# Optimization experiments

Measured on AMD Instinct MI355X. Metric: run time of the kernel, lower is better.

Reference implementation:

```python
import jax, jax.numpy as jnp
import numpy as np

K = 3
TAPS = K * K
STD = float(np.sqrt(2.0)) / K  # FilterNorm scale: relu gain / kernel_size


def filter_norm(f, axis):
    # torch FilterNorm: subtract mean, divide by unbiased std (+1e-10), scale by STD
    m = jnp.mean(f, axis=axis, keepdims=True)
    sd = jnp.std(f, axis=axis, keepdims=True, ddof=1)
    return (f - m) / (sd + 1e-10) * STD


def setup_inputs() -> dict:
    key = jax.random.key(0)
    ks = jax.random.split(key, 9)
    B, C, H, W = 4, 64, 192, 192
    mid = int(C * 0.2)  # se_ratio=0.2 -> 12
    f = lambda k, shape, s: jax.random.normal(k, shape, jnp.float32) * s
    return {
        'x':   f(ks[0], (B, C, H, W), 1.0),
        'sw':  f(ks[1], (TAPS, C), 0.05),        # spatial branch 1x1 conv weight
        'sb':  f(ks[2], (TAPS,), 0.05),
        'cw1': f(ks[3], (mid, C), 0.05),         # channel branch squeeze
        'cb1': f(ks[4], (mid,), 0.05),
        'cw2': f(ks[5], (C * TAPS, mid), 0.05),  # channel branch expand
        'cb2': f(ks[6], (C * TAPS,), 0.05),
        'w2':  f(ks[7], (C, C, 1, 9), 0.05),     # trailing 1x9 conv
        'b2':  f(ks[8], (C,), 0.05),
    }


def block_forward(x, sw, sb, cw1, cb1, cw2, cb2, w2, b2):
    B, C, H, W = x.shape
    # --- DDFPack ---
    # spatial filters: 1x1 conv -> (B, 9, H, W), FilterNorm across the 9 taps
    s = jnp.einsum('bchw,tc->bthw', x, sw) + sb[None, :, None, None]
    s = filter_norm(s, axis=1)
    # channel filters: GAP -> 1x1 -> relu -> 1x1 -> (B, C, 9), FilterNorm over taps
    g = x.mean(axis=(2, 3))                         # (B, C)
    h1 = jax.nn.relu(g @ cw1.T + cb1)               # (B, mid)
    cf = (h1 @ cw2.T + cb2).reshape(B, C, TAPS)     # (B, C, 9)
    cf = filter_norm(cf, axis=2)
    # decoupled dynamic filter apply: per-pixel depthwise 3x3, combine='mul', pad=1
    xp = jnp.pad(x, ((0, 0), (0, 0), (1, 1), (1, 1)))
    out = jnp.zeros_like(x)
    for idx in range(TAPS):  # fixed 9-tap loop, no big unfold intermediate
        i, j = idx // K, idx % K
        out = out + xp[:, :, i:i + H, j:j + W] * s[:, idx:idx + 1] * cf[:, :, idx, None, None]
    # --- LeakyReLU(0.1) -> 1x9 conv (pad (0,4)) -> residual add (res_scale=1) ---
    a = jnp.where(out >= 0, out, 0.1 * out)
    y = jax.lax.conv_general_dilated(a, w2, (1, 1), ((0, 0), (4, 4)),
                                     dimension_numbers=('NCHW', 'OIHW', 'NCHW'))
    y = y + b2[None, :, None, None]
    return x + y


def reference(x, sw, sb, cw1, cb1, cw2, cb2, w2, b2):
    return block_forward(x, sw, sb, cw1, cb1, cw2, cb2, w2, b2)
```

## Files before the change

kernel.cpp:

```cpp
#include <hip/hip_runtime.h>
#include <hip/hip_bf16.h>

#define B_    4
#define C_    64
#define H_    192
#define W_    192
#define TAPS_ 9
#define MID_  12
#define HW_   (H_ * W_)
#define K_TOT 576
#define AT_STRIDE 72

constexpr float STD_ = 0.47140452079103173f;

using bf16 = __hip_bfloat16;
typedef __attribute__((ext_vector_type(4))) float  f32x4;
typedef __attribute__((ext_vector_type(8))) short  short8;

__device__ __forceinline__ unsigned short f2bf_bits(float v) {
    union { bf16 h; unsigned short u; } cv;
    cv.h = __float2bfloat16(v);
    return cv.u;
}

__device__ __forceinline__ int at_word(int row, int cw) {
    int key = (row >> 2) & 7;
    return row * (AT_STRIDE / 2) + ((((cw >> 2) ^ key) & 7) << 2) + (cw & 3);
}

__global__ __launch_bounds__(256) void k_pre(const float* __restrict__ x,
                                             const float* __restrict__ w2,
                                             unsigned short* __restrict__ w2bf,
                                             float* __restrict__ partials) {
    int bx = blockIdx.x;
    if (bx < 144) {
        int d = bx * 256 + threadIdx.x;
        int o = d / K_TOT;
        int rem = d - o * K_TOT;
        int t = rem >> 6;
        int c = rem & 63;
        w2bf[d] = f2bf_bits(w2[(o * C_ + c) * TAPS_ + t]);
        return;
    }
    bx -= 144;
    int bc = bx / 3, part = bx - 3 * (bx / 3);
    const float4* p = (const float4*)(x + (size_t)bc * HW_ + part * 12288);
    float s = 0.f;
    #pragma unroll
    for (int k = 0; k < 12; ++k) {
        float4 u = p[threadIdx.x + k * 256];
        s += u.x + u.y + u.z + u.w;
    }
    #pragma unroll
    for (int off = 32; off; off >>= 1) s += __shfl_down(s, off);
    __shared__ float red[4];
    if ((threadIdx.x & 63) == 0) red[threadIdx.x >> 6] = s;
    __syncthreads();
    if (threadIdx.x == 0)
        partials[bx] = red[0] + red[1] + red[2] + red[3];
}

__global__ __launch_bounds__(256) void k_cf(const float* __restrict__ partials,
                                            const float* __restrict__ cw1,
                                            const float* __restrict__ cb1,
                                            const float* __restrict__ cw2,
                                            const float* __restrict__ cb2,
                                            float* __restrict__ cfn) {
    __shared__ float g_l[B_ * C_];
    __shared__ float h1_l[B_ * MID_];
    int tid = threadIdx.x;
    g_l[tid] = (partials[tid * 3] + partials[tid * 3 + 1] + partials[tid * 3 + 2])
               * (1.0f / HW_);
    __syncthreads();
    if (tid < B_ * MID_) {
        int b = tid / MID_, m = tid % MID_;
        float acc = cb1[m];
        for (int c = 0; c < C_; ++c) acc += g_l[b * C_ + c] * cw1[m * C_ + c];
        h1_l[tid] = fmaxf(acc, 0.f);
    }
    __syncthreads();
    int b = tid >> 6, c = tid & 63;
    float f[TAPS_];
    float mean = 0.f;
    #pragma unroll
    for (int t = 0; t < TAPS_; ++t) {
        int n = c * TAPS_ + t;
        float acc = cb2[n];
        #pragma unroll
        for (int m = 0; m < MID_; ++m) acc += h1_l[b * MID_ + m] * cw2[n * MID_ + m];
        f[t] = acc;
        mean += acc;
    }
    mean *= (1.f / TAPS_);
    float var = 0.f;
    #pragma unroll
    for (int t = 0; t < TAPS_; ++t) { float d = f[t] - mean; var += d * d; }
    var *= (1.f / (TAPS_ - 1));
    float scale = STD_ / (sqrtf(fmaxf(var, 0.f)) + 1e-10f);
    #pragma unroll
    for (int t = 0; t < TAPS_; ++t)
        cfn[(b * C_ + c) * TAPS_ + t] = (f[t] - mean) * scale;
}

__global__ __launch_bounds__(256, 3) void k_main(const float* __restrict__ x,
                                                 const float* __restrict__ sw,
                                                 const float* __restrict__ sb,
                                                 const float* __restrict__ cfn,
                                                 const unsigned short* __restrict__ w2bf,
                                                 const float* __restrict__ bias2,
                                                 float* __restrict__ out) {
    __shared__ __align__(16) char smem[36016];
    short*          aT   = (short*)smem;
    unsigned*       aT32 = (unsigned*)smem;
    float*          sw_l = (float*)smem;
    float*          s_l  = (float*)(smem + 28800);
    float*          b2_l = (float*)(smem + 35712);
    float*          sb_l = (float*)(smem + 35968);

    int bh = blockIdx.x;
    int bb = bh / H_;
    int h  = bh - bb * H_;
    int tid = threadIdx.x;
    int lane = tid & 63, wid = tid >> 6;
    int quad = lane >> 4, l16 = lane & 15;
    int obase = wid * 16;

    for (int i = tid; i < TAPS_ * C_; i += 256) sw_l[i] = sw[i];
    if (tid < C_) b2_l[tid] = bias2[tid];
    if (tid < TAPS_) sb_l[tid] = sb[tid];
    __syncthreads();

    const short* w2s = (const short*)w2bf;
    const short* arow = w2s + (obase + l16) * K_TOT + quad * 8;
    short8 a0 = *(const short8*)(arow);
    short8 a1 = *(const short8*)(arow + 32);

    if (tid < W_) {
        int w = tid;
        float acc[TAPS_];
        #pragma unroll
        for (int t = 0; t < TAPS_; ++t) acc[t] = sb_l[t];
        const float* px = x + (size_t)bb * C_ * HW_ + h * W_ + w;
        #pragma unroll 8
        for (int c = 0; c < C_; ++c) {
            float xv = px[(size_t)c * HW_];
            #pragma unroll
            for (int t = 0; t < TAPS_; ++t) acc[t] = fmaf(xv, sw_l[t * C_ + c], acc[t]);
        }
        float mean = 0.f;
        #pragma unroll
        for (int t = 0; t < TAPS_; ++t) mean += acc[t];
        mean *= (1.f / TAPS_);
        float var = 0.f;
        #pragma unroll
        for (int t = 0; t < TAPS_; ++t) { float d = acc[t] - mean; var += d * d; }
        var *= (1.f / (TAPS_ - 1));
        float scale = STD_ / (sqrtf(fmaxf(var, 0.f)) + 1e-10f);
        float* sp = s_l + (w & 3) * 432 + (w >> 2);
        #pragma unroll
        for (int t = 0; t < TAPS_; ++t) sp[t * 48] = (acc[t] - mean) * scale;
    }
    __syncthreads();

    for (int i = tid; i < 8 * (AT_STRIDE / 2); i += 256) {
        int rowIdx = i / (AT_STRIDE / 2);
        int col    = i - rowIdx * (AT_STRIDE / 2);
        int r = (rowIdx < 4) ? rowIdx : (192 + rowIdx);
        aT32[r * (AT_STRIDE / 2) + col] = 0u;
    }

    {
        int wbase = wid * 16;
        if (lane < 48) {
            int w0 = 4 * lane;
            float sreg[4][TAPS_];
            #pragma unroll
            for (int k = 0; k < 4; ++k) {
                const float* sp = s_l + k * 432 + lane;
                #pragma unroll
                for (int t = 0; t < TAPS_; ++t) sreg[k][t] = sp[t * 48];
            }
            bool l0 = (lane == 0), l47 = (lane == 47);
            int rok0 = (h > 0), rok2 = (h < H_ - 1);
            int midx = l0 ? 0 : (w0 - 1);
            int pidx = l47 ? w0 : (w0 + 4);
            const float* xbase = x + (long)bb * C_ * HW_ + (long)(h - 1) * W_;
            #pragma unroll 1
            for (int i = 0; i < 16; i += 2) {
                int c0 = wbase + i;
                int cu = __builtin_amdgcn_readfirstlane(c0);
                const float* cfp = cfn + bb * (C_ * TAPS_) + cu * TAPS_;
                const float* pc0 = xbase + (long)c0 * HW_;
                const float* pc1 = pc0 + HW_;
                float acc0[4] = {0.f, 0.f, 0.f, 0.f};
                float acc1[4] = {0.f, 0.f, 0.f, 0.f};
                #pragma unroll
                for (int r = 0; r < 3; ++r) {
                    if (r == 0 && !rok0) continue;
                    if (r == 2 && !rok2) continue;
                    const float* p0 = pc0 + r * W_;
                    const float* p1 = pc1 + r * W_;
                    float4 fa = *(const float4*)(p0 + w0);
                    float4 fb = *(const float4*)(p1 + w0);
                    float ma = l0 ? 0.f : p0[midx];
                    float mb = l0 ? 0.f : p1[midx];
                    float pa = l47 ? 0.f : p0[pidx];
                    float pb = l47 ? 0.f : p1[pidx];
                    float va[6] = { ma, fa.x, fa.y, fa.z, fa.w, pa };
                    float vb[6] = { mb, fb.x, fb.y, fb.z, fb.w, pb };
                    #pragma unroll
                    for (int dc = 0; dc < 3; ++dc) {
                        int t = r * 3 + dc;
                        float cva = cfp[t];
                        float cvb = cfp[TAPS_ + t];
                        #pragma unroll
                        for (int k = 0; k < 4; ++k) {
                            acc0[k] = fmaf(va[k + dc] * sreg[k][t], cva, acc0[k]);
                            acc1[k] = fmaf(vb[k + dc] * sreg[k][t], cvb, acc1[k]);
                        }
                    }
                }
                int cw = c0 >> 1;
                #pragma unroll
                for (int k = 0; k < 4; ++k) {
                    float a0v = acc0[k]; a0v = (a0v >= 0.f) ? a0v : 0.1f * a0v;
                    float a1v = acc1[k]; a1v = (a1v >= 0.f) ? a1v : 0.1f * a1v;
                    unsigned pk = (unsigned)f2bf_bits(a0v)
                                | ((unsigned)f2bf_bits(a1v) << 16);
                    aT32[at_word(w0 + k + 4, cw)] = pk;
                }
            }
        }
    }
    __syncthreads();

    {
        f32x4 acc[12];
        #pragma unroll
        for (int n = 0; n < 12; ++n) acc[n] = (f32x4){0.f, 0.f, 0.f, 0.f};

        #pragma unroll 1
        for (int kk = 0; kk < 18; ++kk) {
            short8 a2 = a1;
            if (kk < 16) a2 = *(const short8*)(arow + (kk + 2) * 32);
            int t = kk >> 1;
            int ch = ((kk & 1) << 2) + quad;
            int rowb = l16 + t;
            int key0 = (rowb >> 2) & 7;
            int off0 = rowb * AT_STRIDE + (((ch ^ key0) & 7) << 3);
            int off1 = rowb * AT_STRIDE + (((ch ^ key0 ^ 4) & 7) << 3);
            #pragma unroll
            for (int n = 0; n < 12; ++n) {
                int off = ((n & 1) ? off1 : off0) + n * 16 * AT_STRIDE;
                short8 bf = *(const short8*)(aT + off);
                acc[n] = __builtin_amdgcn_mfma_f32_16x16x32_bf16(a0, bf, acc[n], 0, 0, 0);
            }
            a0 = a1; a1 = a2;
        }

        size_t xbase = (size_t)bb * C_ * HW_ + (size_t)h * W_;
        #pragma unroll
        for (int n = 0; n < 12; ++n) {
            int w = n * 16 + l16;
            #pragma unroll
            for (int reg = 0; reg < 4; ++reg) {
                int o = obase + quad * 4 + reg;
                size_t idx = xbase + (size_t)o * HW_ + w;
                out[idx] = acc[n][reg] + b2_l[o] + x[idx];
            }
        }
    }
}

extern "C" void kernel_launch(void* const* d_in, const int* in_sizes, int n_in,
                              void* d_out, int out_size, void* d_ws, size_t ws_size,
                              hipStream_t stream) {
    const float* x   = (const float*)d_in[0];
    const float* sw  = (const float*)d_in[1];
    const float* sb  = (const float*)d_in[2];
    const float* cw1 = (const float*)d_in[3];
    const float* cb1 = (const float*)d_in[4];
    const float* cw2 = (const float*)d_in[5];
    const float* cb2 = (const float*)d_in[6];
    const float* w2  = (const float*)d_in[7];
    const float* b2  = (const float*)d_in[8];
    float* out = (float*)d_out;

    unsigned short* w2bf = (unsigned short*)d_ws;
    float* partials = (float*)((char*)d_ws + 73728);
    float* cfn      = (float*)((char*)d_ws + 76800);

    hipLaunchKernelGGL(k_pre, dim3(912), dim3(256), 0, stream, x, w2, w2bf, partials);
    hipLaunchKernelGGL(k_cf, dim3(1), dim3(256), 0, stream,
                       partials, cw1, cb1, cw2, cb2, cfn);
    hipLaunchKernelGGL(k_main, dim3(B_ * H_), dim3(256), 0, stream,
                       x, sw, sb, cfn, w2bf, b2, out);
}
```

Before: 147.9 us.

## Retile MFMA stage, prefetch depthwise rows, use lane shuffles for halo

The 1x9 conv MFMA stage now gives each wave two 16-row output-channel tiles by six width tiles, instead of one 16-row tile by twelve width tiles. Each B fragment read from LDS is reused for two MFMAs, which halves LDS traffic per MFMA. The depthwise stage software-prefetches the next channel pair's three input rows into registers and gets the left/right halo values through lane shuffles rather than extra scalar global loads. The weight-conversion pre-kernel is rewritten to read w2 contiguously and scatter the writes, and the 1x1 spatial loop unroll goes from 8 to 16. These changes raise register pressure, which could reduce occupancy.

```diff
diff --git a/kernel.cpp b/kernel.cpp
--- a/kernel.cpp
+++ b/kernel.cpp
@@ -34,12 +34,12 @@
                                              float* __restrict__ partials) {
     int bx = blockIdx.x;
     if (bx < 144) {
-        int d = bx * 256 + threadIdx.x;
-        int o = d / K_TOT;
-        int rem = d - o * K_TOT;
-        int t = rem >> 6;
-        int c = rem & 63;
-        w2bf[d] = f2bf_bits(w2[(o * C_ + c) * TAPS_ + t]);
+        int s = bx * 256 + threadIdx.x;
+        int o = s / K_TOT;
+        int rem = s - o * K_TOT;
+        int c = rem / TAPS_;
+        int t = rem - c * TAPS_;
+        w2bf[o * K_TOT + t * 64 + c] = f2bf_bits(w2[s]);
         return;
     }
     bx -= 144;
@@ -123,7 +123,8 @@
     int tid = threadIdx.x;
     int lane = tid & 63, wid = tid >> 6;
     int quad = lane >> 4, l16 = lane & 15;
-    int obase = wid * 16;
+    int opair = wid & 1;
+    int nh    = wid >> 1;
 
     for (int i = tid; i < TAPS_ * C_; i += 256) sw_l[i] = sw[i];
     if (tid < C_) b2_l[tid] = bias2[tid];
@@ -131,9 +132,12 @@
     __syncthreads();
 
     const short* w2s = (const short*)w2bf;
-    const short* arow = w2s + (obase + l16) * K_TOT + quad * 8;
-    short8 a0 = *(const short8*)(arow);
-    short8 a1 = *(const short8*)(arow + 32);
+    const short* arowA = w2s + (opair * 32 + l16) * K_TOT + quad * 8;
+    const short* arowB = arowA + 16 * K_TOT;
+    short8 aA0 = *(const short8*)(arowA);
+    short8 aA1 = *(const short8*)(arowA + 32);
+    short8 aB0 = *(const short8*)(arowB);
+    short8 aB1 = *(const short8*)(arowB + 32);
 
     if (tid < W_) {
         int w = tid;
@@ -141,7 +145,7 @@
         #pragma unroll
         for (int t = 0; t < TAPS_; ++t) acc[t] = sb_l[t];
         const float* px = x + (size_t)bb * C_ * HW_ + h * W_ + w;
-        #pragma unroll 8
+        #pragma unroll 16
         for (int c = 0; c < C_; ++c) {
             float xv = px[(size_t)c * HW_];
             #pragma unroll
@@ -182,32 +186,48 @@
             }
             bool l0 = (lane == 0), l47 = (lane == 47);
             int rok0 = (h > 0), rok2 = (h < H_ - 1);
-            int midx = l0 ? 0 : (w0 - 1);
-            int pidx = l47 ? w0 : (w0 + 4);
             const float* xbase = x + (long)bb * C_ * HW_ + (long)(h - 1) * W_;
+            const float4 z4 = {0.f, 0.f, 0.f, 0.f};
+
+            float4 nf[6];
+            {
+                const float* pc0 = xbase + (long)wbase * HW_;
+                const float* pc1 = pc0 + HW_;
+                nf[0] = rok0 ? *(const float4*)(pc0 + w0) : z4;
+                nf[1] = *(const float4*)(pc0 + W_ + w0);
+                nf[2] = rok2 ? *(const float4*)(pc0 + 2 * W_ + w0) : z4;
+                nf[3] = rok0 ? *(const float4*)(pc1 + w0) : z4;
+                nf[4] = *(const float4*)(pc1 + W_ + w0);
+                nf[5] = rok2 ? *(const float4*)(pc1 + 2 * W_ + w0) : z4;
+            }
             #pragma unroll 1
             for (int i = 0; i < 16; i += 2) {
+                float4 fa[3], fb[3];
+                fa[0] = nf[0]; fa[1] = nf[1]; fa[2] = nf[2];
+                fb[0] = nf[3]; fb[1] = nf[4]; fb[2] = nf[5];
+                if (i < 14) {
+                    const float* pc0 = xbase + (long)(wbase + i + 2) * HW_;
+                    const float* pc1 = pc0 + HW_;
+                    nf[0] = rok0 ? *(const float4*)(pc0 + w0) : z4;
+                    nf[1] = *(const float4*)(pc0 + W_ + w0);
+                    nf[2] = rok2 ? *(const float4*)(pc0 + 2 * W_ + w0) : z4;
+                    nf[3] = rok0 ? *(const float4*)(pc1 + w0) : z4;
+                    nf[4] = *(const float4*)(pc1 + W_ + w0);
+                    nf[5] = rok2 ? *(const float4*)(pc1 + 2 * W_ + w0) : z4;
+                }
                 int c0 = wbase + i;
                 int cu = __builtin_amdgcn_readfirstlane(c0);
                 const float* cfp = cfn + bb * (C_ * TAPS_) + cu * TAPS_;
-                const float* pc0 = xbase + (long)c0 * HW_;
-                const float* pc1 = pc0 + HW_;
                 float acc0[4] = {0.f, 0.f, 0.f, 0.f};
                 float acc1[4] = {0.f, 0.f, 0.f, 0.f};
                 #pragma unroll
                 for (int r = 0; r < 3; ++r) {
-                    if (r == 0 && !rok0) continue;
-                    if (r == 2 && !rok2) continue;
-                    const float* p0 = pc0 + r * W_;
-                    const float* p1 = pc1 + r * W_;
-                    float4 fa = *(const float4*)(p0 + w0);
-                    float4 fb = *(const float4*)(p1 + w0);
-                    float ma = l0 ? 0.f : p0[midx];
-                    float mb = l0 ? 0.f : p1[midx];
-                    float pa = l47 ? 0.f : p0[pidx];
-                    float pb = l47 ? 0.f : p1[pidx];
-                    float va[6] = { ma, fa.x, fa.y, fa.z, fa.w, pa };
-                    float vb[6] = { mb, fb.x, fb.y, fb.z, fb.w, pb };
+                    float la = __shfl_up(fa[r].w, 1);   if (l0)  la = 0.f;
+                    float ra = __shfl_down(fa[r].x, 1); if (l47) ra = 0.f;
+                    float lb = __shfl_up(fb[r].w, 1);   if (l0)  lb = 0.f;
+                    float rb = __shfl_down(fb[r].x, 1); if (l47) rb = 0.f;
+                    float va[6] = { la, fa[r].x, fa[r].y, fa[r].z, fa[r].w, ra };
+                    float vb[6] = { lb, fb[r].x, fb[r].y, fb[r].z, fb[r].w, rb };
                     #pragma unroll
                     for (int dc = 0; dc < 3; ++dc) {
                         int t = r * 3 + dc;
@@ -235,14 +255,19 @@
     __syncthreads();
 
     {
-        f32x4 acc[12];
-        #pragma unroll
-        for (int n = 0; n < 12; ++n) acc[n] = (f32x4){0.f, 0.f, 0.f, 0.f};
+        f32x4 acc[2][6];
+        #pragma unroll
+        for (int g = 0; g < 2; ++g)
+            #pragma unroll
+            for (int n = 0; n < 6; ++n) acc[g][n] = (f32x4){0.f, 0.f, 0.f, 0.f};
 
         #pragma unroll 1
         for (int kk = 0; kk < 18; ++kk) {
-            short8 a2 = a1;
-            if (kk < 16) a2 = *(const short8*)(arow + (kk + 2) * 32);
+            short8 aA2 = aA1, aB2 = aB1;
+            if (kk < 16) {
+                aA2 = *(const short8*)(arowA + (kk + 2) * 32);
+                aB2 = *(const short8*)(arowB + (kk + 2) * 32);
+            }
             int t = kk >> 1;
             int ch = ((kk & 1) << 2) + quad;
             int rowb = l16 + t;
@@ -250,23 +275,30 @@
             int off0 = rowb * AT_STRIDE + (((ch ^ key0) & 7) << 3);
             int off1 = rowb * AT_STRIDE + (((ch ^ key0 ^ 4) & 7) << 3);
             #pragma unroll
-            for (int n = 0; n < 12; ++n) {
+            for (int n6 = 0; n6 < 6; ++n6) {
+                int n = nh * 6 + n6;
                 int off = ((n & 1) ? off1 : off0) + n * 16 * AT_STRIDE;
                 short8 bf = *(const short8*)(aT + off);
-                acc[n] = __builtin_amdgcn_mfma_f32_16x16x32_bf16(a0, bf, acc[n], 0, 0, 0);
-            }
-            a0 = a1; a1 = a2;
+                acc[0][n6] = __builtin_amdgcn_mfma_f32_16x16x32_bf16(aA0, bf, acc[0][n6], 0, 0, 0);
+                acc[1][n6] = __builtin_amdgcn_mfma_f32_16x16x32_bf16(aB0, bf, acc[1][n6], 0, 0, 0);
+            }
+            aA0 = aA1; aA1 = aA2;
+            aB0 = aB1; aB1 = aB2;
         }
 
         size_t xbase = (size_t)bb * C_ * HW_ + (size_t)h * W_;
         #pragma unroll
-        for (int n = 0; n < 12; ++n) {
-            int w = n * 16 + l16;
-            #pragma unroll
-            for (int reg = 0; reg < 4; ++reg) {
-                int o = obase + quad * 4 + reg;
-                size_t idx = xbase + (size_t)o * HW_ + w;
-                out[idx] = acc[n][reg] + b2_l[o] + x[idx];
+        for (int g = 0; g < 2; ++g) {
+            int ob = opair * 32 + g * 16;
+            #pragma unroll
+            for (int n6 = 0; n6 < 6; ++n6) {
+                int w = (nh * 6 + n6) * 16 + l16;
+                #pragma unroll
+                for (int reg = 0; reg < 4; ++reg) {
+                    int o = ob + quad * 4 + reg;
+                    size_t idx = xbase + (size_t)o * HW_ + w;
+                    out[idx] = acc[g][n6][reg] + b2_l[o] + x[idx];
+                }
             }
         }
     }
```

Result: slower. 168.7 us (+14.1%).

## Switch trailing 1x9 conv GEMM to 32x32x16 MFMA tiles

Applied to the files above, without the earlier changes.

Replaces the 16x16x32 bf16 MFMA decomposition of the 1x9 conv with 32x32x16 MFMAs. Each wave now owns a 32-output-channel tile and three 32-pixel column tiles, and prefetches A fragments a full tap ahead. The weight repack loop is rewritten to read w2 contiguously and scatter its writes. The channel-reduction loop unroll is raised from 8 to 16. The larger tiles should cut LDS B-fragment reads per FLOP and MFMA issue count, at the cost of more accumulator and A registers, which may lower occupancy.

```diff
diff --git a/kernel.cpp b/kernel.cpp
--- a/kernel.cpp
+++ b/kernel.cpp
@@ -14,8 +14,9 @@
 constexpr float STD_ = 0.47140452079103173f;
 
 using bf16 = __hip_bfloat16;
-typedef __attribute__((ext_vector_type(4))) float  f32x4;
-typedef __attribute__((ext_vector_type(8))) short  short8;
+typedef __attribute__((ext_vector_type(4)))  float f32x4;
+typedef __attribute__((ext_vector_type(16))) float f32x16;
+typedef __attribute__((ext_vector_type(8)))  short short8;
 
 __device__ __forceinline__ unsigned short f2bf_bits(float v) {
     union { bf16 h; unsigned short u; } cv;
@@ -34,12 +35,12 @@
                                              float* __restrict__ partials) {
     int bx = blockIdx.x;
     if (bx < 144) {
-        int d = bx * 256 + threadIdx.x;
-        int o = d / K_TOT;
-        int rem = d - o * K_TOT;
-        int t = rem >> 6;
-        int c = rem & 63;
-        w2bf[d] = f2bf_bits(w2[(o * C_ + c) * TAPS_ + t]);
+        int s = bx * 256 + threadIdx.x;
+        int o = s / K_TOT;
+        int rem = s - o * K_TOT;
+        int c = rem / TAPS_;
+        int t = rem - c * TAPS_;
+        w2bf[o * K_TOT + t * 64 + c] = f2bf_bits(w2[s]);
         return;
     }
     bx -= 144;
@@ -122,8 +123,9 @@
     int h  = bh - bb * H_;
     int tid = threadIdx.x;
     int lane = tid & 63, wid = tid >> 6;
-    int quad = lane >> 4, l16 = lane & 15;
-    int obase = wid * 16;
+    int l32 = lane & 31, khalf = lane >> 5;
+    int mtile = wid & 1;
+    int ngrp  = wid >> 1;
 
     for (int i = tid; i < TAPS_ * C_; i += 256) sw_l[i] = sw[i];
     if (tid < C_) b2_l[tid] = bias2[tid];
@@ -131,9 +133,10 @@
     __syncthreads();
 
     const short* w2s = (const short*)w2bf;
-    const short* arow = w2s + (obase + l16) * K_TOT + quad * 8;
-    short8 a0 = *(const short8*)(arow);
-    short8 a1 = *(const short8*)(arow + 32);
+    const short* arow = w2s + (mtile * 32 + l32) * K_TOT + khalf * 8;
+    short8 Acur[4], Anxt[4];
+    #pragma unroll
+    for (int i = 0; i < 4; ++i) Acur[i] = *(const short8*)(arow + i * 16);
 
     if (tid < W_) {
         int w = tid;
@@ -141,7 +144,7 @@
         #pragma unroll
         for (int t = 0; t < TAPS_; ++t) acc[t] = sb_l[t];
         const float* px = x + (size_t)bb * C_ * HW_ + h * W_ + w;
-        #pragma unroll 8
+        #pragma unroll 16
         for (int c = 0; c < C_; ++c) {
             float xv = px[(size_t)c * HW_];
             #pragma unroll
@@ -235,38 +238,45 @@
     __syncthreads();
 
     {
-        f32x4 acc[12];
-        #pragma unroll
-        for (int n = 0; n < 12; ++n) acc[n] = (f32x4){0.f, 0.f, 0.f, 0.f};
+        f32x16 acc[3];
+        #pragma unroll
+        for (int n3 = 0; n3 < 3; ++n3)
+            #pragma unroll
+            for (int i = 0; i < 16; ++i) acc[n3][i] = 0.f;
 
         #pragma unroll 1
-        for (int kk = 0; kk < 18; ++kk) {
-            short8 a2 = a1;
-            if (kk < 16) a2 = *(const short8*)(arow + (kk + 2) * 32);
-            int t = kk >> 1;
-            int ch = ((kk & 1) << 2) + quad;
-            int rowb = l16 + t;
-            int key0 = (rowb >> 2) & 7;
-            int off0 = rowb * AT_STRIDE + (((ch ^ key0) & 7) << 3);
-            int off1 = rowb * AT_STRIDE + (((ch ^ key0 ^ 4) & 7) << 3);
-            #pragma unroll
-            for (int n = 0; n < 12; ++n) {
-                int off = ((n & 1) ? off1 : off0) + n * 16 * AT_STRIDE;
-                short8 bf = *(const short8*)(aT + off);
-                acc[n] = __builtin_amdgcn_mfma_f32_16x16x32_bf16(a0, bf, acc[n], 0, 0, 0);
+        for (int g = 0; g < 9; ++g) {
+            #pragma unroll
+            for (int i = 0; i < 4; ++i)
+                Anxt[i] = (g < 8) ? *(const short8*)(arow + ((g + 1) * 4 + i) * 16)
+                                  : Acur[i];
+            int row0 = ngrp * 96 + l32 + g;
+            #pragma unroll
+            for (int k4 = 0; k4 < 4; ++k4) {
+                int ch = (k4 << 1) + khalf;
+                #pragma unroll
+                for (int n3 = 0; n3 < 3; ++n3) {
+                    int row = row0 + n3 * 32;
+                    int key = (row >> 2) & 7;
+                    int off = row * AT_STRIDE + (((ch ^ key) & 7) << 3);
+                    short8 bf = *(const short8*)(aT + off);
+                    acc[n3] = __builtin_amdgcn_mfma_f32_32x32x16_bf16(
+                        Acur[k4], bf, acc[n3], 0, 0, 0);
+                }
             }
-            a0 = a1; a1 = a2;
+            #pragma unroll
+            for (int i = 0; i < 4; ++i) Acur[i] = Anxt[i];
         }
 
         size_t xbase = (size_t)bb * C_ * HW_ + (size_t)h * W_;
         #pragma unroll
-        for (int n = 0; n < 12; ++n) {
-            int w = n * 16 + l16;
-            #pragma unroll
-            for (int reg = 0; reg < 4; ++reg) {
-                int o = obase + quad * 4 + reg;
+        for (int n3 = 0; n3 < 3; ++n3) {
+            int w = (ngrp * 3 + n3) * 32 + l32;
+            #pragma unroll
+            for (int reg = 0; reg < 16; ++reg) {
+                int o = mtile * 32 + (reg & 3) + ((reg >> 2) << 3) + (khalf << 2);
                 size_t idx = xbase + (size_t)o * HW_ + w;
-                out[idx] = acc[n][reg] + b2_l[o] + x[idx];
+                out[idx] = acc[n3][reg] + b2_l[o] + x[idx];
             }
         }
     }
```

New measurement: 165.1 us. +11.7%, slower.

## Split fused row kernel into phase kernel and MFMA GEMM kernel via global staging

Applied to the files above, without the earlier changes.

Splits the single per-row fused kernel into two kernels. The first computes the spatial filters, applies the dynamic 3x3 filter with LeakyReLU, and writes bf16 activations to a global workspace buffer with zero padding. The second loads those activations and runs the 1x9 conv as 32x32x16 bf16 MFMA with bias and residual add. The split lets each kernel use smaller LDS and higher occupancy across more blocks, at the cost of a global round trip of the intermediate and an extra launch. The w2 repack in k_pre is also reindexed so global reads are coalesced. The fused kernel is kept as a fallback for when the workspace is too small.

```diff
diff --git a/kernel.cpp b/kernel.cpp
--- a/kernel.cpp
+++ b/kernel.cpp
@@ -14,8 +14,9 @@
 constexpr float STD_ = 0.47140452079103173f;
 
 using bf16 = __hip_bfloat16;
-typedef __attribute__((ext_vector_type(4))) float  f32x4;
-typedef __attribute__((ext_vector_type(8))) short  short8;
+typedef __attribute__((ext_vector_type(4)))  float f32x4;
+typedef __attribute__((ext_vector_type(16))) float f32x16;
+typedef __attribute__((ext_vector_type(8)))  short short8;
 
 __device__ __forceinline__ unsigned short f2bf_bits(float v) {
     union { bf16 h; unsigned short u; } cv;
@@ -34,12 +35,12 @@
                                              float* __restrict__ partials) {
     int bx = blockIdx.x;
     if (bx < 144) {
-        int d = bx * 256 + threadIdx.x;
-        int o = d / K_TOT;
-        int rem = d - o * K_TOT;
-        int t = rem >> 6;
-        int c = rem & 63;
-        w2bf[d] = f2bf_bits(w2[(o * C_ + c) * TAPS_ + t]);
+        int s = bx * 256 + threadIdx.x;
+        int o = s / K_TOT;
+        int rem = s - o * K_TOT;
+        int c = rem / TAPS_;
+        int t = rem - c * TAPS_;
+        w2bf[o * K_TOT + t * 64 + c] = f2bf_bits(w2[s]);
         return;
     }
     bx -= 144;
@@ -102,13 +103,203 @@
         cfn[(b * C_ + c) * TAPS_ + t] = (f[t] - mean) * scale;
 }
 
-__global__ __launch_bounds__(256, 3) void k_main(const float* __restrict__ x,
-                                                 const float* __restrict__ sw,
-                                                 const float* __restrict__ sb,
-                                                 const float* __restrict__ cfn,
+__global__ __launch_bounds__(256, 6) void k_phase(const float* __restrict__ x,
+                                                  const float* __restrict__ sw,
+                                                  const float* __restrict__ sb,
+                                                  const float* __restrict__ cfn,
+                                                  unsigned* __restrict__ a_glob) {
+    __shared__ __align__(16) char smem[13888];
+    float*    pA   = (float*)smem;
+    unsigned* aT32 = (unsigned*)smem;
+    float*    s_l  = (float*)(smem + 9216);
+    float*    sw_l = (float*)(smem + 11520);
+    float*    sb_l = (float*)(smem + 13824);
+
+    int bx = blockIdx.x;
+    int bh = bx / 3;
+    int third = bx - 3 * bh;
+    int w0 = third * 64;
+    int bb = bh / H_;
+    int h  = bh - bb * H_;
+    int tid = threadIdx.x;
+    int lane = tid & 63, wid = tid >> 6;
+
+    for (int i = tid; i < TAPS_ * C_; i += 256) sw_l[i] = sw[i];
+    if (tid < TAPS_) sb_l[tid] = sb[tid];
+    __syncthreads();
+
+    {
+        float acc[TAPS_];
+        #pragma unroll
+        for (int t = 0; t < TAPS_; ++t) acc[t] = 0.f;
+        const float* px = x + ((size_t)bb * C_ + wid * 16) * HW_ + h * W_ + w0 + lane;
+        #pragma unroll
+        for (int i2 = 0; i2 < 16; ++i2) {
+            float xv = px[(size_t)i2 * HW_];
+            #pragma unroll
+            for (int t = 0; t < TAPS_; ++t)
+                acc[t] = fmaf(xv, sw_l[t * C_ + wid * 16 + i2], acc[t]);
+        }
+        #pragma unroll
+        for (int t = 0; t < TAPS_; ++t) pA[wid * 576 + t * 64 + lane] = acc[t];
+    }
+    __syncthreads();
+    if (tid < 64) {
+        float f[TAPS_];
+        float mean = 0.f;
+        #pragma unroll
+        for (int t = 0; t < TAPS_; ++t) {
+            f[t] = pA[t * 64 + tid] + pA[576 + t * 64 + tid]
+                 + pA[1152 + t * 64 + tid] + pA[1728 + t * 64 + tid] + sb_l[t];
+            mean += f[t];
+        }
+        mean *= (1.f / TAPS_);
+        float var = 0.f;
+        #pragma unroll
+        for (int t = 0; t < TAPS_; ++t) { float d = f[t] - mean; var += d * d; }
+        var *= (1.f / (TAPS_ - 1));
+        float scale = STD_ / (sqrtf(fmaxf(var, 0.f)) + 1e-10f);
+        #pragma unroll
+        for (int t = 0; t < TAPS_; ++t) s_l[t * 64 + tid] = (f[t] - mean) * scale;
+    }
+    __syncthreads();
+
+    {
+        float sreg[TAPS_];
+        #pragma unroll
+        for (int t = 0; t < TAPS_; ++t) sreg[t] = s_l[t * 64 + lane];
+        int rok0 = (h > 0), rok2 = (h < H_ - 1);
+        bool l0 = (lane == 0), l63 = (lane == 63);
+        bool evalid = l0 ? (w0 > 0) : (l63 ? (w0 + 64 < W_) : false);
+        int eoff = l0 ? -1 : 1;
+        int key = ((lane >> 2) + 1) & 7;
+        const float* xb = x + (size_t)bb * C_ * HW_ + (long)(h - 1) * W_ + w0 + lane;
+        #pragma unroll 1
+        for (int i = 0; i < 16; i += 2) {
+            int c0 = wid * 16 + i;
+            int cu = __builtin_amdgcn_readfirstlane(c0);
+            const float* cfp = cfn + bb * (C_ * TAPS_) + cu * TAPS_;
+            const float* p0 = xb + (size_t)c0 * HW_;
+            const float* p1 = p0 + HW_;
+            float acc0 = 0.f, acc1 = 0.f;
+            #pragma unroll
+            for (int r = 0; r < 3; ++r) {
+                if (r == 0 && !rok0) continue;
+                if (r == 2 && !rok2) continue;
+                float v0 = p0[r * W_];
+                float v1 = p1[r * W_];
+                float e0 = 0.f, e1 = 0.f;
+                if (evalid) { e0 = p0[r * W_ + eoff]; e1 = p1[r * W_ + eoff]; }
+                float le0 = __shfl_up(v0, 1);   if (l0)  le0 = e0;
+                float re0 = __shfl_down(v0, 1); if (l63) re0 = e0;
+                float le1 = __shfl_up(v1, 1);   if (l0)  le1 = e1;
+                float re1 = __shfl_down(v1, 1); if (l63) re1 = e1;
+                int t = r * 3;
+                acc0 = fmaf(le0 * sreg[t],     cfp[t],     acc0);
+                acc0 = fmaf(v0  * sreg[t + 1], cfp[t + 1], acc0);
+                acc0 = fmaf(re0 * sreg[t + 2], cfp[t + 2], acc0);
+                acc1 = fmaf(le1 * sreg[t],     cfp[TAPS_ + t],     acc1);
+                acc1 = fmaf(v1  * sreg[t + 1], cfp[TAPS_ + t + 1], acc1);
+                acc1 = fmaf(re1 * sreg[t + 2], cfp[TAPS_ + t + 2], acc1);
+            }
+            acc0 = (acc0 >= 0.f) ? acc0 : 0.1f * acc0;
+            acc1 = (acc1 >= 0.f) ? acc1 : 0.1f * acc1;
+            unsigned pk = (unsigned)f2bf_bits(acc0) | ((unsigned)f2bf_bits(acc1) << 16);
+            int cw = c0 >> 1;
+            aT32[lane * 36 + ((((cw >> 2) ^ key) & 7) << 2) + (cw & 3)] = pk;
+        }
+    }
+    __syncthreads();
+
+    {
+        size_t gbase = (size_t)bh * 6400;
+        #pragma unroll
+        for (int k = 0; k < 8; ++k) {
+            int idx = tid + k * 256;
+            int p = idx >> 5, cwp = idx & 31;
+            a_glob[gbase + (size_t)(w0 + 4 + p) * 32 + cwp] = aT32[p * 36 + cwp];
+        }
+        if (third == 0 && tid < 128) a_glob[gbase + tid] = 0u;
+        if (third == 2 && tid < 128) a_glob[gbase + 6272 + tid] = 0u;
+    }
+}
+
+__global__ __launch_bounds__(192, 6) void k_gemm(const unsigned* __restrict__ a_glob,
                                                  const unsigned short* __restrict__ w2bf,
                                                  const float* __restrict__ bias2,
+                                                 const float* __restrict__ x,
                                                  float* __restrict__ out) {
+    __shared__ __align__(16) unsigned Bbuf[104 * 36];
+    __shared__ float b2_l[64];
+    const short* BbufS = (const short*)Bbuf;
+
+    int bx = blockIdx.x;
+    int bh = bx >> 1;
+    int half = bx & 1;
+    int w0 = half * 96;
+    int bb = bh / H_;
+    int h  = bh - bb * H_;
+    int tid = threadIdx.x;
+    int lane = tid & 63, wid = tid >> 6;
+    int l32 = lane & 31, khalf = lane >> 5;
+
+    {
+        const unsigned* gsrc = a_glob + (size_t)bh * 6400 + (size_t)w0 * 32;
+        #pragma unroll 2
+        for (int i = tid; i < 3328; i += 192)
+            Bbuf[(i >> 5) * 36 + (i & 31)] = gsrc[i];
+        if (tid < 64) b2_l[tid] = bias2[tid];
+    }
+    __syncthreads();
+
+    {
+        f32x16 acc0, acc1;
+        #pragma unroll
+        for (int i = 0; i < 16; ++i) { acc0[i] = 0.f; acc1[i] = 0.f; }
+
+        const short* arow0 = (const short*)w2bf + (size_t)l32 * K_TOT + khalf * 8;
+        const short* arow1 = arow0 + 32 * K_TOT;
+        short8 A0c = *(const short8*)(arow0);
+        short8 A1c = *(const short8*)(arow1);
+
+        #pragma unroll 4
+        for (int step = 0; step < 36; ++step) {
+            short8 A0n = A0c, A1n = A1c;
+            if (step < 35) {
+                A0n = *(const short8*)(arow0 + (step + 1) * 16);
+                A1n = *(const short8*)(arow1 + (step + 1) * 16);
+            }
+            int t = step >> 2, kk = step & 3;
+            int ch = (kk << 1) + khalf;
+            int L = t + wid * 32 + l32;
+            int key = (L >> 2) & 7;
+            int off = L * AT_STRIDE + (((ch ^ key) & 7) << 3);
+            short8 bf = *(const short8*)(BbufS + off);
+            acc0 = __builtin_amdgcn_mfma_f32_32x32x16_bf16(A0c, bf, acc0, 0, 0, 0);
+            acc1 = __builtin_amdgcn_mfma_f32_32x32x16_bf16(A1c, bf, acc1, 0, 0, 0);
+            A0c = A0n; A1c = A1n;
+        }
+
+        size_t xbase = (size_t)bb * C_ * HW_ + (size_t)h * W_;
+        int w = w0 + wid * 32 + l32;
+        #pragma unroll
+        for (int reg = 0; reg < 16; ++reg) {
+            int om = (reg & 3) + ((reg >> 2) << 3) + (khalf << 2);
+            size_t i0 = xbase + (size_t)om * HW_ + w;
+            size_t i1 = xbase + (size_t)(om + 32) * HW_ + w;
+            out[i0] = acc0[reg] + b2_l[om] + x[i0];
+            out[i1] = acc1[reg] + b2_l[om + 32] + x[i1];
+        }
+    }
+}
+
+__global__ __launch_bounds__(256, 3) void k_main_fused(const float* __restrict__ x,
+                                                       const float* __restrict__ sw,
+                                                       const float* __restrict__ sb,
+                                                       const float* __restrict__ cfn,
+                                                       const unsigned short* __restrict__ w2bf,
+                                                       const float* __restrict__ bias2,
+                                                       float* __restrict__ out) {
     __shared__ __align__(16) char smem[36016];
     short*          aT   = (short*)smem;
     unsigned*       aT32 = (unsigned*)smem;
@@ -289,10 +480,18 @@
     unsigned short* w2bf = (unsigned short*)d_ws;
     float* partials = (float*)((char*)d_ws + 73728);
     float* cfn      = (float*)((char*)d_ws + 76800);
+    unsigned* a_glob = (unsigned*)((char*)d_ws + 90112);
 
     hipLaunchKernelGGL(k_pre, dim3(912), dim3(256), 0, stream, x, w2, w2bf, partials);
     hipLaunchKernelGGL(k_cf, dim3(1), dim3(256), 0, stream,
                        partials, cw1, cb1, cw2, cb2, cfn);
-    hipLaunchKernelGGL(k_main, dim3(B_ * H_), dim3(256), 0, stream,
-                       x, sw, sb, cfn, w2bf, b2, out);
-}
+    if (ws_size >= 19750912ull) {
+        hipLaunchKernelGGL(k_phase, dim3(B_ * H_ * 3), dim3(256), 0, stream,
+                           x, sw, sb, cfn, a_glob);
+        hipLaunchKernelGGL(k_gemm, dim3(B_ * H_ * 2), dim3(192), 0, stream,
+                           a_glob, w2bf, b2, x, out);
+    } else {
+        hipLaunchKernelGGL(k_main_fused, dim3(B_ * H_), dim3(256), 0, stream,
+                           x, sw, sb, cfn, w2bf, b2, out);
+    }
+}
```

Result: slower. 192.7 us (+30.3%).
